# Kernel tuning notes

Measured on AMD Instinct MI355X. Metric: run time of the kernel, lower is better.

## Reference

```python
import jax, jax.numpy as jnp
import numpy as np

NUM_QUERIES = 300


def setup_inputs() -> dict:
    key = jax.random.key(0)
    ks = jax.random.split(key, 16)
    B, C, NC = 16, 256, 80
    s = 0.02
    return {
        "s3": jax.random.normal(ks[0], (B, C, 128, 128), jnp.float32),
        "s4": jax.random.normal(ks[1], (B, C, 64, 64), jnp.float32),
        "s5": jax.random.normal(ks[2], (B, C, 32, 32), jnp.float32),
        "w_score": jax.random.normal(ks[3], (C, NC), jnp.float32) * s,
        "b_score": jnp.zeros((NC,), jnp.float32),
        "w1": jax.random.normal(ks[4], (C, C), jnp.float32) * s,
        "b1": jnp.zeros((C,), jnp.float32),
        "w2": jax.random.normal(ks[5], (C, C), jnp.float32) * s,
        "b2": jnp.zeros((C,), jnp.float32),
        "w3": jax.random.normal(ks[6], (C, 4), jnp.float32) * s,
        "b3": jnp.zeros((4,), jnp.float32),
        "w_proj": jax.random.normal(ks[7], (C, C), jnp.float32) * s,
        "b_proj": jnp.zeros((C,), jnp.float32),
    }


def _flatten(feats):
    # each feat [B,C,H,W] -> [B,H*W,C]; concat over levels
    mems = [f.reshape(f.shape[0], f.shape[1], -1).transpose(0, 2, 1) for f in feats]
    return jnp.concatenate(mems, axis=1)


def reference(s3, s4, s5, w_score, b_score, w1, b1, w2, b2, w3, b3, w_proj, b_proj):
    memory = _flatten([s3, s4, s5])  # [B, N, C]

    # encoder heads
    enc_logits = memory @ w_score + b_score                      # [B, N, num_classes]
    h = jax.nn.relu(memory @ w1 + b1)
    h = jax.nn.relu(h @ w2 + b2)
    enc_boxes = h @ w3 + b3                                      # [B, N, 4]

    # top-k query selection: sigmoid -> per-token max class score -> topk -> gather
    scores = jax.nn.sigmoid(enc_logits).max(axis=-1)             # [B, N]
    topk_scores, topk_idx = jax.lax.top_k(scores, NUM_QUERIES)   # [B, K]
    topk_mem = jnp.take_along_axis(memory, topk_idx[:, :, None], axis=1)    # [B, K, C]
    topk_boxes = jnp.take_along_axis(enc_boxes, topk_idx[:, :, None], axis=1)  # [B, K, 4]

    tgt = topk_mem @ w_proj + b_proj                             # [B, K, C]
    ref_points = jax.nn.sigmoid(topk_boxes)                      # [B, K, 4]

    return (tgt, ref_points, enc_logits, jax.nn.sigmoid(enc_boxes), topk_idx, topk_scores)
```

## Files before the change

### kernel.cpp

```cpp
#include <hip/hip_runtime.h>
#include <math.h>

#define BATCH 16
#define CDIM 256
#define NCLS 80
#define N3 16384
#define N4 4096
#define N5 1024
#define NTOK 21504
#define KQ 300
#define KSEL 512
#define CANDMAX 1024

typedef __attribute__((ext_vector_type(8))) short short8;
typedef __attribute__((ext_vector_type(4))) float floatx4;
typedef unsigned short ushort_t;

__device__ __forceinline__ float sigmoidf_(float x) {
    return 1.0f / (1.0f + __expf(-x));
}

__device__ __forceinline__ ushort_t f2bf(float f) {
    unsigned int x = __float_as_uint(f);
    unsigned int r = (x + 0x7FFFu + ((x >> 16) & 1u)) >> 16;
    return (ushort_t)r;
}

__device__ __forceinline__ void gload16(const void* g, void* l) {
    __builtin_amdgcn_global_load_lds(
        (const __attribute__((address_space(1))) unsigned int*)g,
        (__attribute__((address_space(3))) unsigned int*)l,
        16, 0, 0);
}

__device__ __forceinline__ void locate_level(
    int n, int bb,
    const float* __restrict__ s3, const float* __restrict__ s4, const float* __restrict__ s5,
    const float*& src, int& nloc, int& lsz)
{
    if (n < N3)           { src = s3 + (size_t)bb * CDIM * N3; nloc = n;           lsz = N3; }
    else if (n < N3 + N4) { src = s4 + (size_t)bb * CDIM * N4; nloc = n - N3;      lsz = N4; }
    else                  { src = s5 + (size_t)bb * CDIM * N5; nloc = n - N3 - N4; lsz = N5; }
}

__global__ __launch_bounds__(256) void prep_weights(
    const float* __restrict__ w1, const float* __restrict__ w2,
    const float* __restrict__ w_score,
    ushort_t* __restrict__ w1T, ushort_t* __restrict__ w2T, ushort_t* __restrict__ wsT)
{
    const int k = threadIdx.x;
    const int c = blockIdx.x;
    const int klo = k & 7;
    if (c < 256) {
        const size_t d = (size_t)c * 256 + ((((k >> 3) ^ (c & 7)) << 3) | klo);
        w1T[d] = f2bf(w1[k * 256 + c]);
    } else if (c < 512) {
        const int c2 = c - 256;
        const size_t d = (size_t)c2 * 256 + ((((k >> 3) ^ (c2 & 7)) << 3) | klo);
        w2T[d] = f2bf(w2[k * 256 + c2]);
    } else {
        const int c2 = c - 512;
        const size_t d = (size_t)c2 * 256 + ((((k >> 3) ^ (c2 & 7)) << 3) | klo);
        wsT[d] = (c2 < NCLS) ? f2bf(w_score[k * NCLS + c2]) : (ushort_t)0;
    }
}

__global__ __launch_bounds__(256, 2) void enc_mfma_kernel(
    const float* __restrict__ s3, const float* __restrict__ s4, const float* __restrict__ s5,
    const ushort_t* __restrict__ w1T, const ushort_t* __restrict__ w2T,
    const ushort_t* __restrict__ wsT,
    const float* __restrict__ b_score, const float* __restrict__ b1,
    const float* __restrict__ b2,
    const float* __restrict__ w3, const float* __restrict__ b3,
    float* __restrict__ out_logits, float* __restrict__ out_sboxes,
    float* __restrict__ ws_scores)
{
    __shared__ __align__(16) ushort_t ldsA[256 * 68];
    __shared__ __align__(16) ushort_t wbufL[2][32 * 256];
    __shared__ float bsc_s[96];
    __shared__ float b1_s[256];
    __shared__ float b2_s[256];
    __shared__ __align__(16) float w3_s[256 * 4];

    const int t = threadIdx.x;
    const int lane = t & 63;
    const int w = t >> 6;
    const int ml = lane & 15;
    const int quad = lane >> 4;
    const int kq = quad * 8;
    const int m8 = ml & 7;

    const int bb = blockIdx.x / 336;
    const int tile = blockIdx.x % 336;
    const int T0 = tile * 64;

    auto stage_async = [&](const ushort_t* wg, int dbuf) {
        const char* g = (const char*)wg + w * 1024 + (lane << 4);
        char* l = (char*)&wbufL[dbuf][0] + w * 1024;
        #pragma unroll
        for (int i = 0; i < 4; ++i)
            gload16(g + i * 4096, l + i * 4096);
    };

    stage_async(wsT, 0);

    if (t < 96) bsc_s[t] = b_score[t];
    b1_s[t] = b1[t];
    b2_s[t] = b2[t];
    *(float4*)&w3_s[t * 4] = *(const float4*)(w3 + t * 4);

    const float* src; int nloc, lsz;
    locate_level(T0, bb, s3, s4, s5, src, nloc, lsz);

    {
        const int tokq = t & 15;
        const int kr = t >> 4;
        #pragma unroll
        for (int p = 0; p < 16; ++p) {
            const int k = p * 16 + kr;
            const float4 v = *(const float4*)(src + (size_t)k * lsz + nloc + 4 * tokq);
            const unsigned int lo = (unsigned int)f2bf(v.x) | ((unsigned int)f2bf(v.y) << 16);
            const unsigned int hi = (unsigned int)f2bf(v.z) | ((unsigned int)f2bf(v.w) << 16);
            *(uint2*)&ldsA[k * 68 + 4 * tokq] = make_uint2(lo, hi);
        }
    }
    __syncthreads();

    short8 af[8];
    #pragma unroll
    for (int f = 0; f < 8; ++f) {
        short8 a;
        #pragma unroll
        for (int j = 0; j < 8; ++j)
            a[j] = (short)ldsA[(32 * f + kq + j) * 68 + 16 * w + ml];
        af[f] = a;
    }

    const int tokl0 = 16 * w + quad * 4;
    const int tokg0 = bb * NTOK + T0 + tokl0;

    float smax[4] = {-1e30f, -1e30f, -1e30f, -1e30f};
    float psum[4][4];
    #pragma unroll
    for (int r = 0; r < 4; ++r)
        #pragma unroll
        for (int c = 0; c < 4; ++c) psum[r][c] = 0.f;

    int cur = 0;
    for (int i = 0; i < 19; ++i) {
        if (i + 1 < 19) {
            const int j = i + 1;
            const ushort_t* nxt = (j < 3)  ? (wsT + (size_t)j * 8192)
                                : (j < 11) ? (w1T + (size_t)(j - 3) * 8192)
                                           : (w2T + (size_t)(j - 11) * 8192);
            stage_async(nxt, cur ^ 1);
        }

        if (i == 11) {
            #pragma unroll
            for (int f = 0; f < 8; ++f)
                af[f] = *(const short8*)&ldsA[(16 * w + ml) * 264 + 32 * f + kq];
        }

        const ushort_t* wb = &wbufL[cur][0];
        #pragma unroll
        for (int tt = 0; tt < 2; ++tt) {
            if (i < 3 && (2 * i + tt) >= 5) continue;
            const int row = 16 * tt + ml;
            floatx4 acc = {0.f, 0.f, 0.f, 0.f};
            #pragma unroll
            for (int f = 0; f < 8; ++f) {
                const short8 bf = *(const short8*)&wb[row * 256 + (((4 * f + quad) ^ m8) << 3)];
                acc = __builtin_amdgcn_mfma_f32_16x16x32_bf16(af[f], bf, acc, 0, 0, 0);
            }
            if (i < 3) {
                const int col = 16 * (2 * i + tt) + ml;
                const float bias = bsc_s[col];
                #pragma unroll
                for (int r = 0; r < 4; ++r) {
                    const float v = acc[r] + bias;
                    out_logits[(size_t)(tokg0 + r) * NCLS + col] = v;
                    smax[r] = fmaxf(smax[r], v);
                }
            } else if (i < 11) {
                const int col = 32 * (i - 3) + 16 * tt + ml;
                const float bias = b1_s[col];
                #pragma unroll
                for (int r = 0; r < 4; ++r) {
                    const float v = fmaxf(acc[r] + bias, 0.f);
                    ldsA[(tokl0 + r) * 264 + col] = f2bf(v);
                }
            } else {
                const int col = 32 * (i - 11) + 16 * tt + ml;
                const float bias = b2_s[col];
                const float4 w3v = *(const float4*)&w3_s[col * 4];
                #pragma unroll
                for (int r = 0; r < 4; ++r) {
                    const float v = fmaxf(acc[r] + bias, 0.f);
                    psum[r][0] = fmaf(v, w3v.x, psum[r][0]);
                    psum[r][1] = fmaf(v, w3v.y, psum[r][1]);
                    psum[r][2] = fmaf(v, w3v.z, psum[r][2]);
                    psum[r][3] = fmaf(v, w3v.w, psum[r][3]);
                }
            }
        }

        if (i == 2) {
            #pragma unroll
            for (int r = 0; r < 4; ++r) {
                float m = smax[r];
                m = fmaxf(m, __shfl_xor(m, 1));
                m = fmaxf(m, __shfl_xor(m, 2));
                m = fmaxf(m, __shfl_xor(m, 4));
                m = fmaxf(m, __shfl_xor(m, 8));
                smax[r] = m;
            }
            if (ml == 0) {
                #pragma unroll
                for (int r = 0; r < 4; ++r)
                    ws_scores[bb * NTOK + T0 + 16 * w + quad * 4 + r] = sigmoidf_(smax[r]);
            }
        }

        __syncthreads();
        cur ^= 1;
    }

    #pragma unroll
    for (int r = 0; r < 4; ++r)
        #pragma unroll
        for (int c = 0; c < 4; ++c) {
            float v = psum[r][c];
            v += __shfl_xor(v, 1);
            v += __shfl_xor(v, 2);
            v += __shfl_xor(v, 4);
            v += __shfl_xor(v, 8);
            psum[r][c] = v;
        }
    if (ml == 0) {
        #pragma unroll
        for (int r = 0; r < 4; ++r) {
            float4 o;
            o.x = sigmoidf_(psum[r][0] + b3[0]);
            o.y = sigmoidf_(psum[r][1] + b3[1]);
            o.z = sigmoidf_(psum[r][2] + b3[2]);
            o.w = sigmoidf_(psum[r][3] + b3[3]);
            *(float4*)&out_sboxes[(size_t)(bb * NTOK + T0 + 16 * w + quad * 4 + r) * 4] = o;
        }
    }
}

__global__ __launch_bounds__(256) void select_kernel(
    const float* __restrict__ scores,
    int* __restrict__ cand_idx, unsigned int* __restrict__ cand_cnt)
{
    const int bb = blockIdx.x;
    const int t = threadIdx.x;
    const int lane = t & 63;
    const float* s = scores + bb * NTOK;

    __shared__ unsigned int hist[256];
    __shared__ unsigned int prefix_s, rem_s, cnt_s;

    unsigned int prefix = 0, mask = 0;
    int remaining = KSEL;
    for (int pass = 0; pass < 4; pass++) {
        const int shift = 24 - 8 * pass;
        hist[t] = 0;
        __syncthreads();
        for (int n = t; n < NTOK; n += 256) {
            const unsigned int key = __float_as_uint(s[n]);
            const bool pred = ((key & mask) == prefix);
            const unsigned int bin = pred ? ((key >> shift) & 255u) : 0xFFFFu;
            const unsigned long long alive = __ballot(pred);
            if (alive) {
                const int leader = __builtin_ctzll(alive);
                const unsigned int lbin = (unsigned int)__shfl((int)bin, leader);
                const unsigned long long match = __ballot(pred && bin == lbin);
                if (lane == leader)
                    atomicAdd(&hist[lbin], (unsigned int)__popcll(match));
                else if (pred && bin != lbin)
                    atomicAdd(&hist[bin], 1u);
            }
        }
        __syncthreads();
        if (t == 0) {
            int rem = remaining; unsigned int bsel = 0;
            for (int bin = 255; bin >= 0; bin--) {
                int c = (int)hist[bin];
                if (c >= rem) { bsel = (unsigned int)bin; break; }
                rem -= c;
            }
            prefix_s = prefix | (bsel << shift);
            rem_s = (unsigned int)rem;
        }
        __syncthreads();
        prefix = prefix_s; remaining = (int)rem_s;
        mask |= 0xFFu << shift;
        __syncthreads();
    }
    const unsigned int Tkey = prefix;

    if (t == 0) cnt_s = 0;
    __syncthreads();
    for (int n = t; n < NTOK; n += 256) {
        const unsigned int key = __float_as_uint(s[n]);
        const bool pred = (key >= Tkey);
        const unsigned long long m = __ballot(pred);
        if (m) {
            const int leader = __builtin_ctzll(m);
            unsigned int base = 0;
            if (lane == leader) base = atomicAdd(&cnt_s, (unsigned int)__popcll(m));
            base = (unsigned int)__shfl((int)base, leader);
            if (pred) {
                const unsigned int pos =
                    base + (unsigned int)__popcll(m & ((1ull << lane) - 1ull));
                if (pos < CANDMAX) cand_idx[bb * CANDMAX + pos] = n;
            }
        }
    }
    __syncthreads();
    if (t == 0) {
        unsigned int c = cnt_s; if (c > CANDMAX) c = CANDMAX;
        cand_cnt[bb] = c;
    }
}

__global__ __launch_bounds__(256) void rescore_kernel(
    const float* __restrict__ s3, const float* __restrict__ s4, const float* __restrict__ s5,
    const float* __restrict__ w_score, const float* __restrict__ b_score,
    const int* __restrict__ cand_idx, const unsigned int* __restrict__ cand_cnt,
    double* __restrict__ cand_score, float* __restrict__ cand_mem, int use_cmem)
{
    __shared__ float m_s[CDIM];
    __shared__ double part[256];

    const int t = threadIdx.x;
    const int bb = blockIdx.x / CANDMAX;
    const int cpos = blockIdx.x % CANDMAX;
    if ((unsigned int)cpos >= cand_cnt[bb]) return;

    const int n = cand_idx[bb * CANDMAX + cpos];
    const float* src; int nloc, lsz;
    locate_level(n, bb, s3, s4, s5, src, nloc, lsz);
    m_s[t] = src[(size_t)t * lsz + nloc];
    __syncthreads();

    if (use_cmem)
        cand_mem[((size_t)bb * CANDMAX + cpos) * CDIM + t] = m_s[t];

    const int ks = t >> 7;
    const int c = t & 127;
    double acc = 0.0;
    if (c < NCLS) {
        if (ks == 0) acc = (double)b_score[c];
        const int k0 = 128 * ks;
        for (int k = k0; k < k0 + 128; ++k)
            acc += (double)m_s[k] * (double)w_score[k * NCLS + c];
    }
    part[t] = acc;
    __syncthreads();

    if (t < 128) {
        double tot = (t < NCLS) ? (part[t] + part[t + 128]) : -1.0e300;
        part[t] = tot;
    }
    __syncthreads();

    if (t < 64) {
        double v = fmax(part[t], part[t + 64]);
        v = fmax(v, __shfl_xor(v, 1));
        v = fmax(v, __shfl_xor(v, 2));
        v = fmax(v, __shfl_xor(v, 4));
        v = fmax(v, __shfl_xor(v, 8));
        v = fmax(v, __shfl_xor(v, 16));
        v = fmax(v, __shfl_xor(v, 32));
        if (t == 0) cand_score[bb * CANDMAX + cpos] = v;
    }
}

__global__ __launch_bounds__(512) void fsort_kernel(
    const double* __restrict__ cand_score, const int* __restrict__ cand_idx,
    const unsigned int* __restrict__ cand_cnt,
    float* __restrict__ out_idx_f, float* __restrict__ out_scores,
    int* __restrict__ ws_idx, int* __restrict__ ws_pos)
{
    __shared__ double ss[CANDMAX];
    __shared__ int    ii[CANDMAX];
    __shared__ int    pp[CANDMAX];
    const int bb = blockIdx.x;
    const int t = threadIdx.x;
    const unsigned int cnt = cand_cnt[bb];

    for (int i = t; i < CANDMAX; i += 512) {
        if ((unsigned int)i < cnt) {
            ss[i] = cand_score[bb * CANDMAX + i];
            ii[i] = cand_idx[bb * CANDMAX + i];
        } else {
            ss[i] = -1.0e300;
            ii[i] = 0x7FFFFFFF;
        }
        pp[i] = i;
    }
    __syncthreads();

    for (int ksz = 2; ksz <= CANDMAX; ksz <<= 1) {
        for (int j = ksz >> 1; j > 0; j >>= 1) {
            #pragma unroll
            for (int p = 0; p < CANDMAX / 512; p++) {
                const int i = p * 512 + t;
                const int ixj = i ^ j;
                if (ixj > i) {
                    double sa = ss[i], sb = ss[ixj];
                    int ia = ii[i], ib = ii[ixj];
                    const bool up = ((i & ksz) != 0);
                    const bool agtb = (sa > sb) || (sa == sb && ia < ib);
                    if (agtb == up) {
                        ss[i] = sb; ss[ixj] = sa;
                        ii[i] = ib; ii[ixj] = ia;
                        const int pa = pp[i]; pp[i] = pp[ixj]; pp[ixj] = pa;
                    }
                }
            }
            __syncthreads();
        }
    }

    for (int q = t; q < KQ; q += 512) {
        const double x = ss[q];
        const int idx = ii[q];
        out_scores[bb * KQ + q] = (float)(1.0 / (1.0 + exp(-x)));
        out_idx_f[bb * KQ + q] = (float)idx;
        ws_idx[bb * KQ + q] = idx;
        ws_pos[bb * KQ + q] = pp[q];
    }
}

__global__ __launch_bounds__(256) void gather_proj_kernel(
    const float* __restrict__ s3, const float* __restrict__ s4, const float* __restrict__ s5,
    const float* __restrict__ w_proj, const float* __restrict__ b_proj,
    const int* __restrict__ ws_idx, const int* __restrict__ ws_pos,
    const float* __restrict__ cand_mem, int use_cmem,
    const float* __restrict__ out_sboxes,
    float* __restrict__ out_tgt, float* __restrict__ out_ref)
{
    __shared__ float memQ[20][CDIM];
    __shared__ int qidx[20];
    __shared__ int qpos[20];
    const int t = threadIdx.x;
    const int bb = blockIdx.x / 15;
    const int tile = blockIdx.x % 15;
    const int q0 = tile * 20;

    if (t < 20) {
        qidx[t] = ws_idx[bb * KQ + q0 + t];
        qpos[t] = ws_pos[bb * KQ + q0 + t];
    }
    __syncthreads();

    if (use_cmem) {
        #pragma unroll 4
        for (int q = 0; q < 20; q++)
            memQ[q][t] = cand_mem[((size_t)bb * CANDMAX + qpos[q]) * CDIM + t];
    } else {
        #pragma unroll 4
        for (int q = 0; q < 20; q++) {
            const int n = qidx[q];
            const float* src; int nloc, lsz;
            locate_level(n, bb, s3, s4, s5, src, nloc, lsz);
            memQ[q][t] = src[(size_t)t * lsz + nloc];
        }
    }
    __syncthreads();

    const int j = t;
    float acc[20];
    #pragma unroll
    for (int q = 0; q < 20; q++) acc[q] = b_proj[j];
    for (int k = 0; k < CDIM; k++) {
        const float w = w_proj[(size_t)k * CDIM + j];
        #pragma unroll
        for (int q = 0; q < 20; q++) acc[q] = fmaf(memQ[q][k], w, acc[q]);
    }
    #pragma unroll
    for (int q = 0; q < 20; q++)
        out_tgt[(size_t)(bb * KQ + q0 + q) * CDIM + j] = acc[q];

    if (t < 80) {
        const int q = t >> 2, c = t & 3;
        const int n = qidx[q];
        out_ref[(size_t)(bb * KQ + q0 + q) * 4 + c] =
            out_sboxes[(size_t)(bb * NTOK + n) * 4 + c];
    }
}

extern "C" void kernel_launch(void* const* d_in, const int* in_sizes, int n_in,
                              void* d_out, int out_size, void* d_ws, size_t ws_size,
                              hipStream_t stream) {
    const float* s3      = (const float*)d_in[0];
    const float* s4      = (const float*)d_in[1];
    const float* s5      = (const float*)d_in[2];
    const float* w_score = (const float*)d_in[3];
    const float* b_score = (const float*)d_in[4];
    const float* w1      = (const float*)d_in[5];
    const float* b1      = (const float*)d_in[6];
    const float* w2      = (const float*)d_in[7];
    const float* b2      = (const float*)d_in[8];
    const float* w3      = (const float*)d_in[9];
    const float* b3      = (const float*)d_in[10];
    const float* w_proj  = (const float*)d_in[11];
    const float* b_proj  = (const float*)d_in[12];

    float* out = (float*)d_out;
    float* out_tgt    = out;
    float* out_ref    = out + 1228800;
    float* out_logits = out + 1248000;
    float* out_sboxes = out + 28773120;
    float* out_idx    = out + 30149376;
    float* out_scores = out + 30154176;

    char* ws = (char*)d_ws;
    float*        ws_scores  = (float*)(ws + 0);
    double*       cand_score = (double*)(ws + 1376256);
    int*          cand_idx   = (int*)(ws + 1507328);
    unsigned int* cand_cnt   = (unsigned int*)(ws + 1572864);
    int*          ws_idx     = (int*)(ws + 1573120);
    int*          ws_pos     = (int*)(ws + 1592576);
    ushort_t*     w1T        = (ushort_t*)(ws + 1612032);
    ushort_t*     w2T        = (ushort_t*)(ws + 1743104);
    ushort_t*     wsT        = (ushort_t*)(ws + 1874176);
    float*        cand_mem   = (float*)(ws + 1923328);
    const int use_cmem = (ws_size >= (size_t)1923328 + 16777216) ? 1 : 0;

    prep_weights<<<608, 256, 0, stream>>>(w1, w2, w_score, w1T, w2T, wsT);

    enc_mfma_kernel<<<BATCH * 336, 256, 0, stream>>>(
        s3, s4, s5, w1T, w2T, wsT, b_score, b1, b2, w3, b3,
        out_logits, out_sboxes, ws_scores);

    select_kernel<<<BATCH, 256, 0, stream>>>(ws_scores, cand_idx, cand_cnt);

    rescore_kernel<<<BATCH * CANDMAX, 256, 0, stream>>>(
        s3, s4, s5, w_score, b_score, cand_idx, cand_cnt,
        cand_score, cand_mem, use_cmem);

    fsort_kernel<<<BATCH, 512, 0, stream>>>(
        cand_score, cand_idx, cand_cnt, out_idx, out_scores, ws_idx, ws_pos);

    gather_proj_kernel<<<BATCH * 15, 256, 0, stream>>>(
        s3, s4, s5, w_proj, b_proj, ws_idx, ws_pos, cand_mem, use_cmem,
        out_sboxes, out_tgt, out_ref);
}
```

Measured before the change: 1.020 ms.

## Split waves 2x2 over tokens and columns and swizzle token-major activation LDS

The encoder MFMA kernel changes its wave decomposition. Each wave now covers 32 tokens and one 16-column half, and a single B-fragment feeds two MFMAs, so each weight fragment is read from LDS half as often per MFMA. The input staging now writes a token-major, XOR-swizzled bf16 layout with vector stores, replacing per-element strided A-fragment gathers with 16-byte loads. The score max and box partial sums now combine across column-waves through shared memory, which adds a final barrier and doubles the register footprint for A fragments and accumulators.

```diff
diff --git a/kernel.cpp b/kernel.cpp
--- a/kernel.cpp
+++ b/kernel.cpp
@@ -15,6 +15,8 @@
 typedef __attribute__((ext_vector_type(8))) short short8;
 typedef __attribute__((ext_vector_type(4))) float floatx4;
 typedef unsigned short ushort_t;
+
+#define LA(tok, k) (((tok) * 264) + (((((k) >> 3) ^ ((tok) & 7)) << 3) | ((k) & 7)))
 
 __device__ __forceinline__ float sigmoidf_(float x) {
     return 1.0f / (1.0f + __expf(-x));
@@ -75,24 +77,28 @@
     float* __restrict__ out_logits, float* __restrict__ out_sboxes,
     float* __restrict__ ws_scores)
 {
-    __shared__ __align__(16) ushort_t ldsA[256 * 68];
+    __shared__ __align__(16) ushort_t ldsA[64 * 264];
     __shared__ __align__(16) ushort_t wbufL[2][32 * 256];
-    __shared__ float bsc_s[96];
+    __shared__ float bsc_s[80];
     __shared__ float b1_s[256];
     __shared__ float b2_s[256];
     __shared__ __align__(16) float w3_s[256 * 4];
+    __shared__ float smax_s[2][64];
+    __shared__ __align__(16) float boxp[2][64][4];
 
     const int t = threadIdx.x;
     const int lane = t & 63;
     const int w = t >> 6;
+    const int tw = w & 1;
+    const int cw = w >> 1;
     const int ml = lane & 15;
     const int quad = lane >> 4;
     const int kq = quad * 8;
     const int m8 = ml & 7;
 
     const int bb = blockIdx.x / 336;
-    const int tile = blockIdx.x % 336;
-    const int T0 = tile * 64;
+    const int tile_ = blockIdx.x % 336;
+    const int T0 = tile_ * 64;
 
     auto stage_async = [&](const ushort_t* wg, int dbuf) {
         const char* g = (const char*)wg + w * 1024 + (lane << 4);
@@ -104,7 +110,7 @@
 
     stage_async(wsT, 0);
 
-    if (t < 96) bsc_s[t] = b_score[t];
+    if (t < 80) bsc_s[t] = b_score[t];
     b1_s[t] = b1[t];
     b2_s[t] = b2[t];
     *(float4*)&w3_s[t * 4] = *(const float4*)(w3 + t * 4);
@@ -114,37 +120,50 @@
 
     {
         const int tokq = t & 15;
-        const int kr = t >> 4;
-        #pragma unroll
-        for (int p = 0; p < 16; ++p) {
-            const int k = p * 16 + kr;
-            const float4 v = *(const float4*)(src + (size_t)k * lsz + nloc + 4 * tokq);
-            const unsigned int lo = (unsigned int)f2bf(v.x) | ((unsigned int)f2bf(v.y) << 16);
-            const unsigned int hi = (unsigned int)f2bf(v.z) | ((unsigned int)f2bf(v.w) << 16);
-            *(uint2*)&ldsA[k * 68 + 4 * tokq] = make_uint2(lo, hi);
-        }
-    }
-    __syncthreads();
-
-    short8 af[8];
+        const int kg = t >> 4;
+        #pragma unroll
+        for (int p = 0; p < 2; ++p) {
+            const int kbase = 8 * kg + 128 * p;
+            float4 v[8];
+            #pragma unroll
+            for (int j = 0; j < 8; ++j)
+                v[j] = *(const float4*)(src + (size_t)(kbase + j) * lsz + nloc + 4 * tokq);
+            #pragma unroll
+            for (int r = 0; r < 4; ++r) {
+                short8 a;
+                #pragma unroll
+                for (int j = 0; j < 8; ++j)
+                    a[j] = (short)f2bf(((const float*)&v[j])[r]);
+                *(short8*)&ldsA[LA(4 * tokq + r, kbase)] = a;
+            }
+        }
+    }
+    __syncthreads();
+
+    short8 af[2][8];
     #pragma unroll
-    for (int f = 0; f < 8; ++f) {
-        short8 a;
-        #pragma unroll
-        for (int j = 0; j < 8; ++j)
-            a[j] = (short)ldsA[(32 * f + kq + j) * 68 + 16 * w + ml];
-        af[f] = a;
-    }
-
-    const int tokl0 = 16 * w + quad * 4;
-    const int tokg0 = bb * NTOK + T0 + tokl0;
-
-    float smax[4] = {-1e30f, -1e30f, -1e30f, -1e30f};
-    float psum[4][4];
+    for (int tl = 0; tl < 2; ++tl) {
+        const int tok = 32 * tw + 16 * tl + ml;
+        #pragma unroll
+        for (int f = 0; f < 8; ++f)
+            af[tl][f] = *(const short8*)&ldsA[LA(tok, 32 * f + kq)];
+    }
+
+    const int gtok0 = bb * NTOK + T0;
+
+    float smaxr[2][4];
     #pragma unroll
-    for (int r = 0; r < 4; ++r)
-        #pragma unroll
-        for (int c = 0; c < 4; ++c) psum[r][c] = 0.f;
+    for (int tl = 0; tl < 2; ++tl)
+        #pragma unroll
+        for (int r = 0; r < 4; ++r) smaxr[tl][r] = -1e30f;
+
+    float psum[2][4][4];
+    #pragma unroll
+    for (int tl = 0; tl < 2; ++tl)
+        #pragma unroll
+        for (int r = 0; r < 4; ++r)
+            #pragma unroll
+            for (int c = 0; c < 4; ++c) psum[tl][r][c] = 0.f;
 
     int cur = 0;
     for (int i = 0; i < 19; ++i) {
@@ -158,68 +177,78 @@
 
         if (i == 11) {
             #pragma unroll
-            for (int f = 0; f < 8; ++f)
-                af[f] = *(const short8*)&ldsA[(16 * w + ml) * 264 + 32 * f + kq];
+            for (int tl = 0; tl < 2; ++tl) {
+                const int tok = 32 * tw + 16 * tl + ml;
+                #pragma unroll
+                for (int f = 0; f < 8; ++f)
+                    af[tl][f] = *(const short8*)&ldsA[LA(tok, 32 * f + kq)];
+            }
         }
 
         const ushort_t* wb = &wbufL[cur][0];
-        #pragma unroll
-        for (int tt = 0; tt < 2; ++tt) {
-            if (i < 3 && (2 * i + tt) >= 5) continue;
-            const int row = 16 * tt + ml;
-            floatx4 acc = {0.f, 0.f, 0.f, 0.f};
-            #pragma unroll
-            for (int f = 0; f < 8; ++f) {
-                const short8 bf = *(const short8*)&wb[row * 256 + (((4 * f + quad) ^ m8) << 3)];
-                acc = __builtin_amdgcn_mfma_f32_16x16x32_bf16(af[f], bf, acc, 0, 0, 0);
-            }
-            if (i < 3) {
-                const int col = 16 * (2 * i + tt) + ml;
+        const int row = 16 * cw + ml;
+        floatx4 acc0 = {0.f, 0.f, 0.f, 0.f};
+        floatx4 acc1 = {0.f, 0.f, 0.f, 0.f};
+        #pragma unroll
+        for (int f = 0; f < 8; ++f) {
+            const short8 bf = *(const short8*)&wb[row * 256 + (((4 * f + quad) ^ m8) << 3)];
+            acc0 = __builtin_amdgcn_mfma_f32_16x16x32_bf16(af[0][f], bf, acc0, 0, 0, 0);
+            acc1 = __builtin_amdgcn_mfma_f32_16x16x32_bf16(af[1][f], bf, acc1, 0, 0, 0);
+        }
+
+        if (i < 3) {
+            const int col = 32 * i + 16 * cw + ml;
+            if (col < NCLS) {
                 const float bias = bsc_s[col];
                 #pragma unroll
-                for (int r = 0; r < 4; ++r) {
-                    const float v = acc[r] + bias;
-                    out_logits[(size_t)(tokg0 + r) * NCLS + col] = v;
-                    smax[r] = fmaxf(smax[r], v);
-                }
-            } else if (i < 11) {
-                const int col = 32 * (i - 3) + 16 * tt + ml;
-                const float bias = b1_s[col];
+                for (int tl = 0; tl < 2; ++tl)
+                    #pragma unroll
+                    for (int r = 0; r < 4; ++r) {
+                        const float v = (tl ? acc1[r] : acc0[r]) + bias;
+                        const int ltok = 32 * tw + 16 * tl + 4 * quad + r;
+                        out_logits[(size_t)(gtok0 + ltok) * NCLS + col] = v;
+                        smaxr[tl][r] = fmaxf(smaxr[tl][r], v);
+                    }
+            }
+            if (i == 2) {
+                #pragma unroll
+                for (int tl = 0; tl < 2; ++tl)
+                    #pragma unroll
+                    for (int r = 0; r < 4; ++r) {
+                        float m = smaxr[tl][r];
+                        m = fmaxf(m, __shfl_xor(m, 1));
+                        m = fmaxf(m, __shfl_xor(m, 2));
+                        m = fmaxf(m, __shfl_xor(m, 4));
+                        m = fmaxf(m, __shfl_xor(m, 8));
+                        if (ml == 0)
+                            smax_s[cw][32 * tw + 16 * tl + 4 * quad + r] = m;
+                    }
+            }
+        } else if (i < 11) {
+            const int col = 32 * (i - 3) + 16 * cw + ml;
+            const float bias = b1_s[col];
+            #pragma unroll
+            for (int tl = 0; tl < 2; ++tl)
                 #pragma unroll
                 for (int r = 0; r < 4; ++r) {
-                    const float v = fmaxf(acc[r] + bias, 0.f);
-                    ldsA[(tokl0 + r) * 264 + col] = f2bf(v);
+                    const float v = fmaxf((tl ? acc1[r] : acc0[r]) + bias, 0.f);
+                    const int ltok = 32 * tw + 16 * tl + 4 * quad + r;
+                    ldsA[LA(ltok, col)] = f2bf(v);
                 }
-            } else {
-                const int col = 32 * (i - 11) + 16 * tt + ml;
-                const float bias = b2_s[col];
-                const float4 w3v = *(const float4*)&w3_s[col * 4];
+        } else {
+            const int col = 32 * (i - 11) + 16 * cw + ml;
+            const float bias = b2_s[col];
+            const float4 w3v = *(const float4*)&w3_s[col * 4];
+            #pragma unroll
+            for (int tl = 0; tl < 2; ++tl)
                 #pragma unroll
                 for (int r = 0; r < 4; ++r) {
-                    const float v = fmaxf(acc[r] + bias, 0.f);
-                    psum[r][0] = fmaf(v, w3v.x, psum[r][0]);
-                    psum[r][1] = fmaf(v, w3v.y, psum[r][1]);
-                    psum[r][2] = fmaf(v, w3v.z, psum[r][2]);
-                    psum[r][3] = fmaf(v, w3v.w, psum[r][3]);
+                    const float v = fmaxf((tl ? acc1[r] : acc0[r]) + bias, 0.f);
+                    psum[tl][r][0] = fmaf(v, w3v.x, psum[tl][r][0]);
+                    psum[tl][r][1] = fmaf(v, w3v.y, psum[tl][r][1]);
+                    psum[tl][r][2] = fmaf(v, w3v.z, psum[tl][r][2]);
+                    psum[tl][r][3] = fmaf(v, w3v.w, psum[tl][r][3]);
                 }
-            }
-        }
-
-        if (i == 2) {
-            #pragma unroll
-            for (int r = 0; r < 4; ++r) {
-                float m = smax[r];
-                m = fmaxf(m, __shfl_xor(m, 1));
-                m = fmaxf(m, __shfl_xor(m, 2));
-                m = fmaxf(m, __shfl_xor(m, 4));
-                m = fmaxf(m, __shfl_xor(m, 8));
-                smax[r] = m;
-            }
-            if (ml == 0) {
-                #pragma unroll
-                for (int r = 0; r < 4; ++r)
-                    ws_scores[bb * NTOK + T0 + 16 * w + quad * 4 + r] = sigmoidf_(smax[r]);
-            }
         }
 
         __syncthreads();
@@ -227,26 +256,31 @@
     }
 
     #pragma unroll
-    for (int r = 0; r < 4; ++r)
-        #pragma unroll
-        for (int c = 0; c < 4; ++c) {
-            float v = psum[r][c];
-            v += __shfl_xor(v, 1);
-            v += __shfl_xor(v, 2);
-            v += __shfl_xor(v, 4);
-            v += __shfl_xor(v, 8);
-            psum[r][c] = v;
-        }
-    if (ml == 0) {
+    for (int tl = 0; tl < 2; ++tl)
         #pragma unroll
         for (int r = 0; r < 4; ++r) {
-            float4 o;
-            o.x = sigmoidf_(psum[r][0] + b3[0]);
-            o.y = sigmoidf_(psum[r][1] + b3[1]);
-            o.z = sigmoidf_(psum[r][2] + b3[2]);
-            o.w = sigmoidf_(psum[r][3] + b3[3]);
-            *(float4*)&out_sboxes[(size_t)(bb * NTOK + T0 + 16 * w + quad * 4 + r) * 4] = o;
-        }
+            float4 pv;
+            float* pva = (float*)&pv;
+            #pragma unroll
+            for (int c = 0; c < 4; ++c) {
+                float v = psum[tl][r][c];
+                v += __shfl_xor(v, 1);
+                v += __shfl_xor(v, 2);
+                v += __shfl_xor(v, 4);
+                v += __shfl_xor(v, 8);
+                pva[c] = v;
+            }
+            if (ml == 0)
+                *(float4*)&boxp[cw][32 * tw + 16 * tl + 4 * quad + r][0] = pv;
+        }
+    __syncthreads();
+
+    if (t < 64)
+        ws_scores[gtok0 + t] = sigmoidf_(fmaxf(smax_s[0][t], smax_s[1][t]));
+    {
+        const int tok = t >> 2, c = t & 3;
+        const float bx = boxp[0][tok][c] + boxp[1][tok][c] + b3[c];
+        out_sboxes[(size_t)(gtok0 + tok) * 4 + c] = sigmoidf_(bx);
     }
 }
 
```

Measured after the change: 991.7 us. 2.8% less time.
